# Performance work log

Measured on AMD Instinct MI355X. Metric: run time of the kernel, lower is better.

## Reference

```python
import jax, jax.numpy as jnp
import numpy as np

N_NODES = 100000
N_EDGES = 1200000
IN_F = 64
OUT_F = 64


def setup_inputs() -> dict:
    key = jax.random.key(0)
    ks = jax.random.split(key, 8)
    rows = jax.random.randint(ks[0], (N_EDGES,), 0, N_NODES)
    cols = jax.random.randint(ks[1], (N_EDGES,), 0, N_NODES)
    vals = jax.random.uniform(ks[2], (N_EDGES,), dtype=jnp.float32)
    features = jax.random.normal(ks[3], (N_NODES, IN_F), dtype=jnp.float32)
    W1 = jax.random.normal(ks[4], (IN_F, OUT_F), dtype=jnp.float32) / np.sqrt(IN_F)
    b1 = jax.random.normal(ks[5], (OUT_F,), dtype=jnp.float32) * 0.01
    W2 = jax.random.normal(ks[6], (IN_F, OUT_F), dtype=jnp.float32) / np.sqrt(IN_F)
    b2 = jax.random.normal(ks[7], (OUT_F,), dtype=jnp.float32) * 0.01
    return {"rows": rows, "cols": cols, "vals": vals, "features": features,
            "W1": W1, "b1": b1, "W2": W2, "b2": b2}


def _spmm(rows, cols, vals, x):
    # y[r] = sum_{e: rows[e]==r} vals[e] * x[cols[e]]  -- COO SpMM via gather + segment_sum
    msgs = vals[:, None] * x[cols]  # [E, F]
    return jax.ops.segment_sum(msgs, rows, num_segments=N_NODES)


def reference(rows, cols, vals, features, W1, b1, W2, b2):
    # L1 = laplacian + selfLoop(identity)  =>  L1 @ X = L @ X + X
    agg1 = _spmm(rows, cols, vals, features) + features          # [N, inF]
    inter_feature = features * features                           # elementwise square
    agg2 = _spmm(rows, cols, vals, inter_feature)                 # [N, inF]
    part1 = agg1 @ W1 + b1                                        # linear
    part2 = agg2 @ W2 + b2                                        # interActTransform
    return part1 + part2
```

## Files before the change

### kernel.cpp

```cpp
#include <hip/hip_runtime.h>


#define ROWS_PER_BUCKET 128
#define ROW_SHIFT 7
#define NBUCK_PAD 784
#define SCAN_T 196
#define CAP 2048
#define CHUNK 4096
#define SCT 512
#define EPT 8
#define MAXB 2048
#define COL_BITS 17
#define COL_MASK 0x1FFFF
#define OVF_CAP 65536

typedef __attribute__((ext_vector_type(8))) short bf16x8;
typedef __attribute__((ext_vector_type(4))) float f32x4;

__device__ __forceinline__ unsigned short f2bf(float x) {
    unsigned u = __float_as_uint(x);
    unsigned r = (u + 0x7FFFu + ((u >> 16) & 1u)) >> 16;
    return (unsigned short)r;
}
__device__ __forceinline__ float bf2f(unsigned short h) {
    return __uint_as_float(((unsigned)h) << 16);
}

__global__ __launch_bounds__(256) void node_transform(
    const float* __restrict__ X, const float* __restrict__ W1,
    const float* __restrict__ b1, const float* __restrict__ W2,
    const float* __restrict__ b2, unsigned short* __restrict__ Yb,
    float* __restrict__ Z, int n_nodes,
    int* __restrict__ gcursor, int* __restrict__ ovf_count)
{
    const int tid = threadIdx.x;

    if (gcursor) {
        int gi = blockIdx.x * 256 + tid;
        if (gi < NBUCK_PAD) gcursor[gi] = gi * CAP;
        if (gi == 0) *ovf_count = 0;
    }

    const int lane = tid & 63;
    const int wave = tid >> 6;
    const int lg = lane >> 4;
    const int lr = lane & 15;

    const int base = blockIdx.x * 128 + wave * 32;

    bf16x8 bw1[2][4];
    bf16x8 bw2[2][4];
#pragma unroll
    for (int ks = 0; ks < 2; ++ks) {
#pragma unroll
        for (int cf = 0; cf < 4; ++cf) {
            const int col = cf * 16 + lr;
            const int k0 = ks * 32 + lg * 8;
            bf16x8 t1, t2;
#pragma unroll
            for (int j = 0; j < 8; ++j) {
                t1[j] = (short)f2bf(W1[(k0 + j) * 64 + col]);
                t2[j] = (short)f2bf(W2[(k0 + j) * 64 + col]);
            }
            bw1[ks][cf] = t1;
            bw2[ks][cf] = t2;
        }
    }

    f32x4 acc1[2][4];
    f32x4 acc2[2][4];
#pragma unroll
    for (int rf = 0; rf < 2; ++rf)
#pragma unroll
        for (int cf = 0; cf < 4; ++cf) {
            acc1[rf][cf] = (f32x4){0.f, 0.f, 0.f, 0.f};
            acc2[rf][cf] = (f32x4){0.f, 0.f, 0.f, 0.f};
        }

#pragma unroll
    for (int rf = 0; rf < 2; ++rf) {
        const int row = base + rf * 16 + lr;
        const bool rok = row < n_nodes;
        const float* xp = X + (size_t)row * 64 + lg * 8;
#pragma unroll
        for (int ks = 0; ks < 2; ++ks) {
            float xv[8];
            if (rok) {
                float4 v0 = *(const float4*)(xp + ks * 32);
                float4 v1 = *(const float4*)(xp + ks * 32 + 4);
                xv[0] = v0.x; xv[1] = v0.y; xv[2] = v0.z; xv[3] = v0.w;
                xv[4] = v1.x; xv[5] = v1.y; xv[6] = v1.z; xv[7] = v1.w;
            } else {
#pragma unroll
                for (int j = 0; j < 8; ++j) xv[j] = 0.f;
            }
            bf16x8 a, q;
#pragma unroll
            for (int j = 0; j < 8; ++j) {
                a[j] = (short)f2bf(xv[j]);
                float s = xv[j] * xv[j];
                q[j] = (short)f2bf(s);
            }
#pragma unroll
            for (int cf = 0; cf < 4; ++cf) {
                acc1[rf][cf] = __builtin_amdgcn_mfma_f32_16x16x32_bf16(
                    a, bw1[ks][cf], acc1[rf][cf], 0, 0, 0);
                acc2[rf][cf] = __builtin_amdgcn_mfma_f32_16x16x32_bf16(
                    q, bw2[ks][cf], acc2[rf][cf], 0, 0, 0);
            }
        }
    }

    float bsv[4];
#pragma unroll
    for (int cf = 0; cf < 4; ++cf)
        bsv[cf] = b1[cf * 16 + lr] + b2[cf * 16 + lr];

#pragma unroll
    for (int rf = 0; rf < 2; ++rf) {
#pragma unroll
        for (int i = 0; i < 4; ++i) {
            const int row = base + rf * 16 + lg * 4 + i;
            if (row < n_nodes) {
#pragma unroll
                for (int cf = 0; cf < 4; ++cf) {
                    const float v1 = acc1[rf][cf][i];
                    const float y = v1 + acc2[rf][cf][i];
                    const float z = v1 + bsv[cf];
                    Yb[(size_t)row * 64 + cf * 16 + lr] = f2bf(y);
                    Z[(size_t)row * 64 + cf * 16 + lr] = z;
                }
            }
        }
    }
}


__global__ __launch_bounds__(512) void bin_scatter(
    const int* __restrict__ rows, const int* __restrict__ cols,
    const float* __restrict__ vals, int* __restrict__ gcursor,
    int2* __restrict__ packed, int* __restrict__ ovf_count,
    int4* __restrict__ ovf, int n_edges) {
    __shared__ int lcount[NBUCK_PAD];
    __shared__ int lstart[NBUCK_PAD];
    __shared__ int gbase[NBUCK_PAD];
    __shared__ int2 sxy[CHUNK];
    __shared__ unsigned short sbk[CHUNK];
    __shared__ int wsum[8];

    int tid = threadIdx.x;
    int eb0 = blockIdx.x * CHUNK;
    int cnt = min(CHUNK, n_edges - eb0);

    for (int k = tid; k < NBUCK_PAD; k += SCT) lcount[k] = 0;
    __syncthreads();

    int eb_[EPT], ep_[EPT], ex_[EPT], ey_[EPT];
#pragma unroll
    for (int t = 0; t < EPT; ++t) {
        int i = tid + SCT * t;
        if (i < cnt) {
            int r = rows[eb0 + i];
            int b = r >> ROW_SHIFT;
            eb_[t] = b;
            ep_[t] = atomicAdd(&lcount[b], 1);
            ex_[t] = ((r & (ROWS_PER_BUCKET - 1)) << COL_BITS) | cols[eb0 + i];
            ey_[t] = __float_as_int(vals[eb0 + i]);
        } else {
            eb_[t] = -1; ep_[t] = 0; ex_[t] = 0; ey_[t] = 0;
        }
    }
    __syncthreads();

    int c0 = 0, c1 = 0, c2 = 0, c3 = 0, psum = 0;
    if (tid < SCAN_T) {
        c0 = lcount[tid * 4 + 0]; c1 = lcount[tid * 4 + 1];
        c2 = lcount[tid * 4 + 2]; c3 = lcount[tid * 4 + 3];
        psum = c0 + c1 + c2 + c3;
    }
    const int lane = tid & 63;
    const int wv = tid >> 6;
    int incl = psum;
#pragma unroll
    for (int o = 1; o < 64; o <<= 1) {
        int n = __shfl_up(incl, o);
        if (lane >= o) incl += n;
    }
    if (lane == 63) wsum[wv] = incl;
    __syncthreads();
    int wpre = 0;
#pragma unroll
    for (int w = 0; w < 7; ++w)
        if (w < wv) wpre += wsum[w];
    int base0 = wpre + incl - psum;
    if (tid < SCAN_T) {
        lstart[tid * 4 + 0] = base0;
        lstart[tid * 4 + 1] = base0 + c0;
        lstart[tid * 4 + 2] = base0 + c0 + c1;
        lstart[tid * 4 + 3] = base0 + c0 + c1 + c2;
    }
    __syncthreads();

    for (int k = tid; k < NBUCK_PAD; k += SCT) {
        if (lcount[k] > 0) gbase[k] = atomicAdd(&gcursor[k], lcount[k]);
    }

#pragma unroll
    for (int t = 0; t < EPT; ++t) {
        if (eb_[t] >= 0) {
            int p = lstart[eb_[t]] + ep_[t];
            sxy[p] = make_int2(ex_[t], ey_[t]);
            sbk[p] = (unsigned short)eb_[t];
        }
    }
    __syncthreads();

    for (int i = tid; i < cnt; i += SCT) {
        int b = sbk[i];
        int2 a = sxy[i];
        int dest = gbase[b] + (i - lstart[b]);
        if (dest < (b + 1) * CAP) {
            packed[dest] = a;
        } else {
            int p = atomicAdd(ovf_count, 1);
            if (p < OVF_CAP)
                ovf[p] = make_int4(b * ROWS_PER_BUCKET + (a.x >> COL_BITS),
                                   a.x & COL_MASK, a.y, 0);
        }
    }
}

__global__ __launch_bounds__(256) void bucket_gather_quads(
    const int* __restrict__ gcursor, const int2* __restrict__ packed,
    const unsigned short* __restrict__ Yb, float* __restrict__ out,
    int n_nodes) {
    __shared__ int2 sxy[MAXB];
    __shared__ int hist[ROWS_PER_BUCKET];
    __shared__ int chs[ROWS_PER_BUCKET];
    __shared__ int chc[ROWS_PER_BUCKET];

    int tid = threadIdx.x;
    int bucket = blockIdx.x >> 1;
    int rhalf = (blockIdx.x & 1) * 64;
    int fquad = tid & 15;
    int grp = tid >> 4;
    int s = bucket * CAP;
    int e = min(gcursor[bucket], s + CAP);
    int row0 = bucket * ROWS_PER_BUCKET;
    const uint2* __restrict__ Y64 = (const uint2*)Yb;

    for (int cb = s; cb < e; cb += MAXB) {
        int cnt = min(MAXB, e - cb);

        if (tid < ROWS_PER_BUCKET) hist[tid] = 0;
        __syncthreads();

        for (int i = tid; i < cnt; i += 256)
            atomicAdd(&hist[packed[cb + i].x >> COL_BITS], 1);
        __syncthreads();

        if (tid < ROWS_PER_BUCKET) chs[tid] = hist[tid];
        __syncthreads();
#pragma unroll
        for (int o = 1; o < ROWS_PER_BUCKET; o <<= 1) {
            int t = 0;
            if (tid < ROWS_PER_BUCKET && tid >= o) t = chs[tid - o];
            __syncthreads();
            if (tid < ROWS_PER_BUCKET) chs[tid] += t;
            __syncthreads();
        }
        if (tid < ROWS_PER_BUCKET) {
            int excl = chs[tid] - hist[tid];
            chs[tid] = excl;
            chc[tid] = excl;
        }
        __syncthreads();

        for (int i = tid; i < cnt; i += 256) {
            int2 a = packed[cb + i];
            int p = atomicAdd(&chc[a.x >> COL_BITS], 1);
            sxy[p] = a;
        }
        __syncthreads();

        for (int rr = 0; rr < 4; ++rr) {
            int r = rhalf + grp * 4 + rr;
            int rc = hist[r];
            int node = row0 + r;
            if (rc == 0 || node >= n_nodes) continue;
            int rs = chs[r];
            float a0 = 0.f, a1 = 0.f, a2 = 0.f, a3 = 0.f;
            int j = 0;
            for (; j + 4 <= rc; j += 4) {
                int2 e0 = sxy[rs + j + 0], e1 = sxy[rs + j + 1];
                int2 e2 = sxy[rs + j + 2], e3 = sxy[rs + j + 3];
                uint2 u0 = Y64[(size_t)(e0.x & COL_MASK) * 16 + fquad];
                uint2 u1 = Y64[(size_t)(e1.x & COL_MASK) * 16 + fquad];
                uint2 u2 = Y64[(size_t)(e2.x & COL_MASK) * 16 + fquad];
                uint2 u3 = Y64[(size_t)(e3.x & COL_MASK) * 16 + fquad];
                float v0 = __int_as_float(e0.y), v1 = __int_as_float(e1.y);
                float v2 = __int_as_float(e2.y), v3 = __int_as_float(e3.y);
                a0 = fmaf(v0, __uint_as_float(u0.x << 16), a0);
                a1 = fmaf(v0, __uint_as_float(u0.x & 0xFFFF0000u), a1);
                a2 = fmaf(v0, __uint_as_float(u0.y << 16), a2);
                a3 = fmaf(v0, __uint_as_float(u0.y & 0xFFFF0000u), a3);
                a0 = fmaf(v1, __uint_as_float(u1.x << 16), a0);
                a1 = fmaf(v1, __uint_as_float(u1.x & 0xFFFF0000u), a1);
                a2 = fmaf(v1, __uint_as_float(u1.y << 16), a2);
                a3 = fmaf(v1, __uint_as_float(u1.y & 0xFFFF0000u), a3);
                a0 = fmaf(v2, __uint_as_float(u2.x << 16), a0);
                a1 = fmaf(v2, __uint_as_float(u2.x & 0xFFFF0000u), a1);
                a2 = fmaf(v2, __uint_as_float(u2.y << 16), a2);
                a3 = fmaf(v2, __uint_as_float(u2.y & 0xFFFF0000u), a3);
                a0 = fmaf(v3, __uint_as_float(u3.x << 16), a0);
                a1 = fmaf(v3, __uint_as_float(u3.x & 0xFFFF0000u), a1);
                a2 = fmaf(v3, __uint_as_float(u3.y << 16), a2);
                a3 = fmaf(v3, __uint_as_float(u3.y & 0xFFFF0000u), a3);
            }
            for (; j < rc; ++j) {
                int2 e0 = sxy[rs + j];
                uint2 u0 = Y64[(size_t)(e0.x & COL_MASK) * 16 + fquad];
                float v0 = __int_as_float(e0.y);
                a0 = fmaf(v0, __uint_as_float(u0.x << 16), a0);
                a1 = fmaf(v0, __uint_as_float(u0.x & 0xFFFF0000u), a1);
                a2 = fmaf(v0, __uint_as_float(u0.y << 16), a2);
                a3 = fmaf(v0, __uint_as_float(u0.y & 0xFFFF0000u), a3);
            }
            float4* op = (float4*)(out + (size_t)node * 64 + fquad * 4);
            float4 o = *op;
            o.x += a0; o.y += a1; o.z += a2; o.w += a3;
            *op = o;
        }
        __syncthreads();
    }
}

__global__ __launch_bounds__(256) void overflow_scatter(
    const int* __restrict__ ovf_count, const int4* __restrict__ ovf,
    const unsigned short* __restrict__ Yb, float* __restrict__ out) {
    int cnt = min(*ovf_count, OVF_CAP);
    long long total = (long long)cnt * 64;
    for (long long i = blockIdx.x * 256 + threadIdx.x; i < total;
         i += (long long)gridDim.x * 256) {
        int e = (int)(i >> 6), f = (int)(i & 63);
        int4 a = ovf[e];
        atomicAdd(&out[(size_t)a.x * 64 + f],
                  __int_as_float(a.z) * bf2f(Yb[(size_t)a.y * 64 + f]));
    }
}


__global__ __launch_bounds__(256) void edge_scatter(
    const int* __restrict__ rows, const int* __restrict__ cols,
    const float* __restrict__ vals, const unsigned short* __restrict__ Yb,
    float* __restrict__ out, int n_edges)
{
    int t = blockIdx.x * 256 + threadIdx.x;
    int e = t >> 4;
    int f = (t & 15) << 2;
    if (e >= n_edges) return;
    int r = rows[e];
    int c = cols[e];
    float v = vals[e];
    const unsigned short* y = Yb + (size_t)c * 64 + f;
    float* o = out + (size_t)r * 64 + f;
    atomicAdd(o + 0, v * bf2f(y[0]));
    atomicAdd(o + 1, v * bf2f(y[1]));
    atomicAdd(o + 2, v * bf2f(y[2]));
    atomicAdd(o + 3, v * bf2f(y[3]));
}

extern "C" void kernel_launch(void* const* d_in, const int* in_sizes, int n_in,
                              void* d_out, int out_size, void* d_ws, size_t ws_size,
                              hipStream_t stream) {
    const int*   rows = (const int*)d_in[0];
    const int*   cols = (const int*)d_in[1];
    const float* vals = (const float*)d_in[2];
    const float* X    = (const float*)d_in[3];
    const float* W1   = (const float*)d_in[4];
    const float* b1   = (const float*)d_in[5];
    const float* W2   = (const float*)d_in[6];
    const float* b2   = (const float*)d_in[7];
    float* out = (float*)d_out;

    const int n_edges = in_sizes[0];
    const int n_nodes = in_sizes[3] / 64;
    const int nbuck = (n_nodes + ROWS_PER_BUCKET - 1) / ROWS_PER_BUCKET;

    char* ws = (char*)d_ws;
    size_t o_Yb     = 0;
    size_t o_packed = o_Yb + (size_t)n_nodes * 64 * 2;
    size_t o_ovf    = o_packed + (size_t)NBUCK_PAD * CAP * 8;
    size_t o_gcurs  = o_ovf + (size_t)OVF_CAP * 16;
    size_t o_ovfcnt = o_gcurs + NBUCK_PAD * 4;
    size_t need     = o_ovfcnt + 16;

    unsigned short* Yb = (unsigned short*)(ws + o_Yb);

    const bool fastpath =
        ws_size >= need && nbuck <= NBUCK_PAD && n_nodes <= (1 << COL_BITS);

    int2* packed  = (int2*)(ws + o_packed);
    int4* ovf     = (int4*)(ws + o_ovf);
    int*  gcursor = fastpath ? (int*)(ws + o_gcurs) : (int*)0;
    int*  ovfcnt  = (int*)(ws + o_ovfcnt);

    int nblocks = (n_nodes + 127) / 128;
    node_transform<<<nblocks, 256, 0, stream>>>(X, W1, b1, W2, b2, Yb, out,
                                                n_nodes, gcursor, ovfcnt);

    if (fastpath) {
        int eb = (n_edges + CHUNK - 1) / CHUNK;
        bin_scatter<<<eb, SCT, 0, stream>>>(rows, cols, vals, gcursor, packed,
                                            ovfcnt, ovf, n_edges);
        bucket_gather_quads<<<nbuck * 2, 256, 0, stream>>>(gcursor, packed, Yb,
                                                           out, n_nodes);
        overflow_scatter<<<128, 256, 0, stream>>>(ovfcnt, ovf, Yb, out);
    } else {
        long long threads = (long long)n_edges * 16;
        int eblocks = (int)((threads + 255) / 256);
        edge_scatter<<<eblocks, 256, 0, stream>>>(rows, cols, vals, Yb, out, n_edges);
    }
}
```

Measured before the change: 155.3 us.

## Precompute bf16 transposed weights, fold overflow scatter into gather kernel, stage edges in LDS

A small prep kernel now converts W1/W2 to transposed bf16 and sums the biases once, so each node_transform block does vector loads instead of 64 strided scalar loads and conversions per lane. The separate overflow_scatter launch is merged into bucket_gather_quads as extra trailing blocks, which removes one kernel launch. The gather kernel also caches the packed edges in LDS during the histogram pass so the second pass does not reload them from global memory, at the cost of an extra 16KB of shared memory per block that may lower occupancy.

```diff
diff --git a/kernel.cpp b/kernel.cpp
--- a/kernel.cpp
+++ b/kernel.cpp
@@ -10,6 +10,7 @@
 #define SCT 512
 #define EPT 8
 #define MAXB 2048
+#define OVF_BLOCKS 64
 #define COL_BITS 17
 #define COL_MASK 0x1FFFF
 #define OVF_CAP 65536
@@ -26,21 +27,32 @@
     return __uint_as_float(((unsigned)h) << 16);
 }
 
+__global__ __launch_bounds__(256) void prep(
+    const float* __restrict__ W1, const float* __restrict__ W2,
+    const float* __restrict__ b1, const float* __restrict__ b2,
+    unsigned short* __restrict__ Wb1t, unsigned short* __restrict__ Wb2t,
+    float* __restrict__ bsum, int* __restrict__ gcursor,
+    int* __restrict__ ovf_count)
+{
+    int i = blockIdx.x * 256 + threadIdx.x;
+    if (gcursor) {
+        if (i < NBUCK_PAD) gcursor[i] = i * CAP;
+        if (i == 0) *ovf_count = 0;
+    }
+    if (i < 64) bsum[i] = b1[i] + b2[i];
+    if (i < 4096) {
+        int col = i >> 6, k = i & 63;
+        Wb1t[col * 64 + k] = f2bf(W1[k * 64 + col]);
+        Wb2t[col * 64 + k] = f2bf(W2[k * 64 + col]);
+    }
+}
+
 __global__ __launch_bounds__(256) void node_transform(
-    const float* __restrict__ X, const float* __restrict__ W1,
-    const float* __restrict__ b1, const float* __restrict__ W2,
-    const float* __restrict__ b2, unsigned short* __restrict__ Yb,
-    float* __restrict__ Z, int n_nodes,
-    int* __restrict__ gcursor, int* __restrict__ ovf_count)
+    const float* __restrict__ X, const unsigned short* __restrict__ Wb1t,
+    const unsigned short* __restrict__ Wb2t, const float* __restrict__ bsum,
+    unsigned short* __restrict__ Yb, float* __restrict__ Z, int n_nodes)
 {
     const int tid = threadIdx.x;
-
-    if (gcursor) {
-        int gi = blockIdx.x * 256 + tid;
-        if (gi < NBUCK_PAD) gcursor[gi] = gi * CAP;
-        if (gi == 0) *ovf_count = 0;
-    }
-
     const int lane = tid & 63;
     const int wave = tid >> 6;
     const int lg = lane >> 4;
@@ -54,16 +66,9 @@
     for (int ks = 0; ks < 2; ++ks) {
 #pragma unroll
         for (int cf = 0; cf < 4; ++cf) {
-            const int col = cf * 16 + lr;
-            const int k0 = ks * 32 + lg * 8;
-            bf16x8 t1, t2;
-#pragma unroll
-            for (int j = 0; j < 8; ++j) {
-                t1[j] = (short)f2bf(W1[(k0 + j) * 64 + col]);
-                t2[j] = (short)f2bf(W2[(k0 + j) * 64 + col]);
-            }
-            bw1[ks][cf] = t1;
-            bw2[ks][cf] = t2;
+            const int off = (cf * 16 + lr) * 64 + ks * 32 + lg * 8;
+            bw1[ks][cf] = *(const bf16x8*)(Wb1t + off);
+            bw2[ks][cf] = *(const bf16x8*)(Wb2t + off);
         }
     }
 
@@ -114,7 +119,7 @@
     float bsv[4];
 #pragma unroll
     for (int cf = 0; cf < 4; ++cf)
-        bsv[cf] = b1[cf * 16 + lr] + b2[cf * 16 + lr];
+        bsv[cf] = bsum[cf * 16 + lr];
 
 #pragma unroll
     for (int rf = 0; rf < 2; ++rf) {
@@ -233,13 +238,31 @@
 __global__ __launch_bounds__(256) void bucket_gather_quads(
     const int* __restrict__ gcursor, const int2* __restrict__ packed,
     const unsigned short* __restrict__ Yb, float* __restrict__ out,
-    int n_nodes) {
+    int n_nodes, const int* __restrict__ ovf_count,
+    const int4* __restrict__ ovf) {
+    __shared__ int2 sraw[MAXB];
     __shared__ int2 sxy[MAXB];
     __shared__ int hist[ROWS_PER_BUCKET];
     __shared__ int chs[ROWS_PER_BUCKET];
     __shared__ int chc[ROWS_PER_BUCKET];
 
     int tid = threadIdx.x;
+    int nbuck2 = ((n_nodes + 127) >> 7) * 2;
+
+    if (blockIdx.x >= (unsigned)nbuck2) {
+        int bo = blockIdx.x - nbuck2;
+        int cnt = min(*ovf_count, OVF_CAP);
+        long long total = (long long)cnt * 64;
+        for (long long i = (long long)bo * 256 + tid; i < total;
+             i += (long long)OVF_BLOCKS * 256) {
+            int e = (int)(i >> 6), f = (int)(i & 63);
+            int4 a = ovf[e];
+            atomicAdd(&out[(size_t)a.x * 64 + f],
+                      __int_as_float(a.z) * bf2f(Yb[(size_t)a.y * 64 + f]));
+        }
+        return;
+    }
+
     int bucket = blockIdx.x >> 1;
     int rhalf = (blockIdx.x & 1) * 64;
     int fquad = tid & 15;
@@ -255,8 +278,11 @@
         if (tid < ROWS_PER_BUCKET) hist[tid] = 0;
         __syncthreads();
 
-        for (int i = tid; i < cnt; i += 256)
-            atomicAdd(&hist[packed[cb + i].x >> COL_BITS], 1);
+        for (int i = tid; i < cnt; i += 256) {
+            int2 a = packed[cb + i];
+            sraw[i] = a;
+            atomicAdd(&hist[a.x >> COL_BITS], 1);
+        }
         __syncthreads();
 
         if (tid < ROWS_PER_BUCKET) chs[tid] = hist[tid];
@@ -277,7 +303,7 @@
         __syncthreads();
 
         for (int i = tid; i < cnt; i += 256) {
-            int2 a = packed[cb + i];
+            int2 a = sraw[i];
             int p = atomicAdd(&chc[a.x >> COL_BITS], 1);
             sxy[p] = a;
         }
@@ -335,20 +361,6 @@
     }
 }
 
-__global__ __launch_bounds__(256) void overflow_scatter(
-    const int* __restrict__ ovf_count, const int4* __restrict__ ovf,
-    const unsigned short* __restrict__ Yb, float* __restrict__ out) {
-    int cnt = min(*ovf_count, OVF_CAP);
-    long long total = (long long)cnt * 64;
-    for (long long i = blockIdx.x * 256 + threadIdx.x; i < total;
-         i += (long long)gridDim.x * 256) {
-        int e = (int)(i >> 6), f = (int)(i & 63);
-        int4 a = ovf[e];
-        atomicAdd(&out[(size_t)a.x * 64 + f],
-                  __int_as_float(a.z) * bf2f(Yb[(size_t)a.y * 64 + f]));
-    }
-}
-
 
 __global__ __launch_bounds__(256) void edge_scatter(
     const int* __restrict__ rows, const int* __restrict__ cols,
@@ -393,12 +405,20 @@
     size_t o_ovf    = o_packed + (size_t)NBUCK_PAD * CAP * 8;
     size_t o_gcurs  = o_ovf + (size_t)OVF_CAP * 16;
     size_t o_ovfcnt = o_gcurs + NBUCK_PAD * 4;
-    size_t need     = o_ovfcnt + 16;
+    size_t o_wb1    = o_ovfcnt + 16;
+    size_t o_wb2    = o_wb1 + 64 * 64 * 2;
+    size_t o_bs     = o_wb2 + 64 * 64 * 2;
+    size_t need     = o_bs + 64 * 4;
 
     unsigned short* Yb = (unsigned short*)(ws + o_Yb);
 
     const bool fastpath =
         ws_size >= need && nbuck <= NBUCK_PAD && n_nodes <= (1 << COL_BITS);
+
+    size_t fb_wb1 = o_Yb + (size_t)n_nodes * 64 * 2;
+    unsigned short* Wb1t = (unsigned short*)(ws + (fastpath ? o_wb1 : fb_wb1));
+    unsigned short* Wb2t = Wb1t + 64 * 64;
+    float* bsum = (float*)(Wb2t + 64 * 64);
 
     int2* packed  = (int2*)(ws + o_packed);
     int4* ovf     = (int4*)(ws + o_ovf);
@@ -406,16 +426,18 @@
     int*  ovfcnt  = (int*)(ws + o_ovfcnt);
 
     int nblocks = (n_nodes + 127) / 128;
-    node_transform<<<nblocks, 256, 0, stream>>>(X, W1, b1, W2, b2, Yb, out,
-                                                n_nodes, gcursor, ovfcnt);
+
+    prep<<<16, 256, 0, stream>>>(W1, W2, b1, b2, Wb1t, Wb2t, bsum,
+                                 gcursor, fastpath ? ovfcnt : (int*)0);
+    node_transform<<<nblocks, 256, 0, stream>>>(X, Wb1t, Wb2t, bsum,
+                                                Yb, out, n_nodes);
 
     if (fastpath) {
         int eb = (n_edges + CHUNK - 1) / CHUNK;
         bin_scatter<<<eb, SCT, 0, stream>>>(rows, cols, vals, gcursor, packed,
                                             ovfcnt, ovf, n_edges);
-        bucket_gather_quads<<<nbuck * 2, 256, 0, stream>>>(gcursor, packed, Yb,
-                                                           out, n_nodes);
-        overflow_scatter<<<128, 256, 0, stream>>>(ovfcnt, ovf, Yb, out);
+        bucket_gather_quads<<<nbuck * 2 + OVF_BLOCKS, 256, 0, stream>>>(
+            gcursor, packed, Yb, out, n_nodes, ovfcnt, ovf);
     } else {
         long long threads = (long long)n_edges * 16;
         int eblocks = (int)((threads + 255) / 256);
```

New measurement: 165.7 us. +6.7%, slower.
